# Kernel tuning notes

Hardware: AMD Instinct MI355X
Metric: run time of the kernel (lower is better)

Reference implementation:

```python
import jax, jax.numpy as jnp
import numpy as np

GAMMA = 1.0

def setup_inputs() -> dict:
    key = jax.random.key(0)
    kx, ky = jax.random.split(key)
    X = jax.random.normal(kx, (8192, 64), dtype=jnp.float32)
    Y = jax.random.normal(ky, (8192, 64), dtype=jnp.float32)
    return {"X": X, "Y": Y}

def reference(X, Y):
    x2 = jnp.sum(X * X, axis=-1)            # (n,)
    y2 = jnp.sum(Y * Y, axis=-1)            # (m,)
    xy = X @ Y.T                            # (n, m)
    dist2 = x2[:, None] + y2[None, :] - 2.0 * xy
    dist2 = jnp.maximum(dist2, 0.0)         # numerical guard
    return jnp.exp(-GAMMA * dist2)
```

## Files before the change

### kernel.cpp

```cpp
#include <hip/hip_runtime.h>

typedef __attribute__((ext_vector_type(8))) short          short8_t;
typedef __attribute__((ext_vector_type(8))) unsigned short ushort8_t;
typedef __attribute__((ext_vector_type(4))) float          floatx4;

constexpr int N_ROWS = 8192;
constexpr int DIM    = 64;
constexpr int TILE   = 128;
constexpr int PANEL  = TILE * DIM;

__device__ __forceinline__ unsigned short bf16_rne(float f) {
    unsigned int u = __float_as_uint(f);
    u += 0x7FFFu + ((u >> 16) & 1u);
    return (unsigned short)(u >> 16);
}

typedef __attribute__((address_space(1))) unsigned int gu32;
typedef __attribute__((address_space(3))) unsigned int lu32;
__device__ __forceinline__ void gload16(const void* g, void* l) {
    __builtin_amdgcn_global_load_lds((gu32*)g, (lu32*)l, 16, 0, 0);
}

__global__ void __launch_bounds__(256)
split_norms_kernel(const float* __restrict__ X, const float* __restrict__ Y,
                   float* __restrict__ x2, float* __restrict__ y2,
                   unsigned short* __restrict__ Xs, unsigned short* __restrict__ Ys) {
    const int r  = blockIdx.x * 256 + threadIdx.x;
    const int p  = r >> 7;
    const int rl = r & 127;
    const int swz = (rl & 7) * 8;
    const size_t pb = (size_t)p * (2 * PANEL);

    const float4* xr = reinterpret_cast<const float4*>(X + (size_t)r * DIM);
    const float4* yr = reinterpret_cast<const float4*>(Y + (size_t)r * DIM);

    float sx = 0.f, sy = 0.f;
#pragma unroll
    for (int c = 0; c < 8; ++c) {
        const int off = (rl * DIM + c * 8) ^ swz;
        float f[8];
        ushort8_t hi, lo;

        *reinterpret_cast<float4*>(&f[0]) = xr[2 * c];
        *reinterpret_cast<float4*>(&f[4]) = xr[2 * c + 1];
#pragma unroll
        for (int e = 0; e < 8; ++e) {
            sx = fmaf(f[e], f[e], sx);
            unsigned short hh = bf16_rne(f[e]);
            hi[e] = hh;
            lo[e] = bf16_rne(f[e] - __uint_as_float((unsigned int)hh << 16));
        }
        *reinterpret_cast<ushort8_t*>(&Xs[pb + off])         = hi;
        *reinterpret_cast<ushort8_t*>(&Xs[pb + PANEL + off]) = lo;

        *reinterpret_cast<float4*>(&f[0]) = yr[2 * c];
        *reinterpret_cast<float4*>(&f[4]) = yr[2 * c + 1];
#pragma unroll
        for (int e = 0; e < 8; ++e) {
            sy = fmaf(f[e], f[e], sy);
            unsigned short hh = bf16_rne(f[e]);
            hi[e] = hh;
            lo[e] = bf16_rne(f[e] - __uint_as_float((unsigned int)hh << 16));
        }
        *reinterpret_cast<ushort8_t*>(&Ys[pb + off])         = hi;
        *reinterpret_cast<ushort8_t*>(&Ys[pb + PANEL + off]) = lo;
    }
    x2[r] = sx;
    y2[r] = sy;
}

__global__ void __launch_bounds__(256, 2)
rbf_mfma_kernel(const unsigned short* __restrict__ Xs,
                const unsigned short* __restrict__ Ys,
                const float* __restrict__ x2, const float* __restrict__ y2,
                float* __restrict__ out) {
    __shared__ unsigned short smem[4 * PANEL];

    const int tid  = threadIdx.x;
    const int lane = tid & 63;
    const int w    = tid >> 6;
    const int row0 = blockIdx.y * TILE;
    const int col0 = blockIdx.x * TILE;

    {
        const unsigned short* src =
            (w < 2) ? Xs + (size_t)blockIdx.y * (2 * PANEL) + w * PANEL
                    : Ys + (size_t)blockIdx.x * (2 * PANEL) + (w & 1) * PANEL;
        unsigned short* dst = &smem[w * PANEL];
#pragma unroll
        for (int it = 0; it < 16; ++it)
            gload16(src + it * 512 + lane * 8, dst + it * 512);
    }
    __syncthreads();

    const int li = lane & 15;
    const int lg = lane >> 4;
    const int wr = (w >> 1) * 64;
    const int wc = (w & 1) * 64;

    floatx4 acc[4][4] = {};

#define LDF(qbase, rowbase, koff)                                              \
    (*reinterpret_cast<const short8_t*>(                                       \
        &smem[(qbase) + ((rowbase) + li) * DIM + (koff)]))

#pragma unroll
    for (int ks = 0; ks < 2; ++ks) {
        const int koff = (ks * 32 + lg * 8) ^ ((li & 7) * 8);
        short8_t aH[4], bH[4], aL[4], bL[4];
#pragma unroll
        for (int mi = 0; mi < 4; ++mi) aH[mi] = LDF(0 * PANEL, wr + mi * 16, koff);
#pragma unroll
        for (int ni = 0; ni < 4; ++ni) bH[ni] = LDF(2 * PANEL, wc + ni * 16, koff);
#pragma unroll
        for (int mi = 0; mi < 4; ++mi)
#pragma unroll
            for (int ni = 0; ni < 4; ++ni)
                acc[mi][ni] = __builtin_amdgcn_mfma_f32_16x16x32_bf16(
                    bH[ni], aH[mi], acc[mi][ni], 0, 0, 0);
#pragma unroll
        for (int ni = 0; ni < 4; ++ni) bL[ni] = LDF(3 * PANEL, wc + ni * 16, koff);
#pragma unroll
        for (int mi = 0; mi < 4; ++mi)
#pragma unroll
            for (int ni = 0; ni < 4; ++ni)
                acc[mi][ni] = __builtin_amdgcn_mfma_f32_16x16x32_bf16(
                    bL[ni], aH[mi], acc[mi][ni], 0, 0, 0);
#pragma unroll
        for (int mi = 0; mi < 4; ++mi) aL[mi] = LDF(1 * PANEL, wr + mi * 16, koff);
#pragma unroll
        for (int mi = 0; mi < 4; ++mi)
#pragma unroll
            for (int ni = 0; ni < 4; ++ni)
                acc[mi][ni] = __builtin_amdgcn_mfma_f32_16x16x32_bf16(
                    bH[ni], aL[mi], acc[mi][ni], 0, 0, 0);
    }
#undef LDF

    const int orow = row0 + wr + li;
    const int ocol = col0 + wc + lg * 4;
#pragma unroll
    for (int mi = 0; mi < 4; ++mi) {
        const float xs = x2[orow + mi * 16];
        float* obase = out + (size_t)(orow + mi * 16) * N_ROWS + ocol;
#pragma unroll
        for (int ni = 0; ni < 4; ++ni) {
            const float4 yv = *reinterpret_cast<const float4*>(&y2[ocol + ni * 16]);
            float4 o;
            o.x = __expf(-fmaxf(fmaf(-2.f, acc[mi][ni][0], xs + yv.x), 0.f));
            o.y = __expf(-fmaxf(fmaf(-2.f, acc[mi][ni][1], xs + yv.y), 0.f));
            o.z = __expf(-fmaxf(fmaf(-2.f, acc[mi][ni][2], xs + yv.z), 0.f));
            o.w = __expf(-fmaxf(fmaf(-2.f, acc[mi][ni][3], xs + yv.w), 0.f));
            *reinterpret_cast<float4*>(obase + ni * 16) = o;
        }
    }
}

extern "C" void kernel_launch(void* const* d_in, const int* in_sizes, int n_in,
                              void* d_out, int out_size, void* d_ws, size_t ws_size,
                              hipStream_t stream) {
    const float* X = (const float*)d_in[0];
    const float* Y = (const float*)d_in[1];
    float* out = (float*)d_out;

    float* x2 = (float*)d_ws;
    float* y2 = x2 + N_ROWS;
    unsigned short* Xs = (unsigned short*)(y2 + N_ROWS);
    unsigned short* Ys = Xs + (N_ROWS / TILE) * 2 * PANEL;

    split_norms_kernel<<<N_ROWS / 256, 256, 0, stream>>>(X, Y, x2, y2, Xs, Ys);

    dim3 grid(N_ROWS / TILE, N_ROWS / TILE);
    rbf_mfma_kernel<<<grid, 256, 0, stream>>>(Xs, Ys, x2, y2, out);
}
```

Before: 76.11 us.

## Pre-pack split bf16 operands in MFMA fragment order and load directly from global

The split kernel now writes the hi/lo bf16 panels in the exact per-lane MFMA fragment order and uses two threads per row, reducing the squared norm with a shuffle. The main kernel drops LDS staging and __syncthreads. It becomes a single-wave 64x64 block that reads fragments straight from global memory as coalesced 16-byte loads. This removes LDS traffic and barriers, at the cost of more global and L2 reads, since operand panels are no longer shared across four waves, and a four-times-larger grid.

```diff
diff --git a/kernel.cpp b/kernel.cpp
--- a/kernel.cpp
+++ b/kernel.cpp
@@ -6,8 +6,7 @@
 
 constexpr int N_ROWS = 8192;
 constexpr int DIM    = 64;
-constexpr int TILE   = 128;
-constexpr int PANEL  = TILE * DIM;
+constexpr int PANEL  = 128 * DIM;
 
 __device__ __forceinline__ unsigned short bf16_rne(float f) {
     unsigned int u = __float_as_uint(f);
@@ -15,29 +14,26 @@
     return (unsigned short)(u >> 16);
 }
 
-typedef __attribute__((address_space(1))) unsigned int gu32;
-typedef __attribute__((address_space(3))) unsigned int lu32;
-__device__ __forceinline__ void gload16(const void* g, void* l) {
-    __builtin_amdgcn_global_load_lds((gu32*)g, (lu32*)l, 16, 0, 0);
-}
-
 __global__ void __launch_bounds__(256)
 split_norms_kernel(const float* __restrict__ X, const float* __restrict__ Y,
                    float* __restrict__ x2, float* __restrict__ y2,
                    unsigned short* __restrict__ Xs, unsigned short* __restrict__ Ys) {
-    const int r  = blockIdx.x * 256 + threadIdx.x;
+    const int t  = blockIdx.x * 256 + threadIdx.x;
+    const int r  = t >> 1;
+    const int h  = t & 1;
     const int p  = r >> 7;
     const int rl = r & 127;
-    const int swz = (rl & 7) * 8;
+    const int g  = rl >> 4;
+    const int li = rl & 15;
     const size_t pb = (size_t)p * (2 * PANEL);
 
-    const float4* xr = reinterpret_cast<const float4*>(X + (size_t)r * DIM);
-    const float4* yr = reinterpret_cast<const float4*>(Y + (size_t)r * DIM);
+    const float4* xr = reinterpret_cast<const float4*>(X + (size_t)r * DIM + h * 32);
+    const float4* yr = reinterpret_cast<const float4*>(Y + (size_t)r * DIM + h * 32);
 
     float sx = 0.f, sy = 0.f;
 #pragma unroll
-    for (int c = 0; c < 8; ++c) {
-        const int off = (rl * DIM + c * 8) ^ swz;
+    for (int c = 0; c < 4; ++c) {
+        const int off = ((g * 2 + h) * 64 + c * 16 + li) * 8;
         float f[8];
         ushort8_t hi, lo;
 
@@ -65,53 +61,37 @@
         *reinterpret_cast<ushort8_t*>(&Ys[pb + off])         = hi;
         *reinterpret_cast<ushort8_t*>(&Ys[pb + PANEL + off]) = lo;
     }
-    x2[r] = sx;
-    y2[r] = sy;
+    sx += __shfl_xor(sx, 1);
+    sy += __shfl_xor(sy, 1);
+    if (h == 0) { x2[r] = sx; y2[r] = sy; }
 }
 
-__global__ void __launch_bounds__(256, 2)
+__global__ void __launch_bounds__(64)
 rbf_mfma_kernel(const unsigned short* __restrict__ Xs,
                 const unsigned short* __restrict__ Ys,
                 const float* __restrict__ x2, const float* __restrict__ y2,
                 float* __restrict__ out) {
-    __shared__ unsigned short smem[4 * PANEL];
-
-    const int tid  = threadIdx.x;
-    const int lane = tid & 63;
-    const int w    = tid >> 6;
-    const int row0 = blockIdx.y * TILE;
-    const int col0 = blockIdx.x * TILE;
-
-    {
-        const unsigned short* src =
-            (w < 2) ? Xs + (size_t)blockIdx.y * (2 * PANEL) + w * PANEL
-                    : Ys + (size_t)blockIdx.x * (2 * PANEL) + (w & 1) * PANEL;
-        unsigned short* dst = &smem[w * PANEL];
-#pragma unroll
-        for (int it = 0; it < 16; ++it)
-            gload16(src + it * 512 + lane * 8, dst + it * 512);
-    }
-    __syncthreads();
-
-    const int li = lane & 15;
-    const int lg = lane >> 4;
-    const int wr = (w >> 1) * 64;
-    const int wc = (w & 1) * 64;
+    const int lane = threadIdx.x;
+    const int row0 = blockIdx.y * 64;
+    const int col0 = blockIdx.x * 64;
+    const unsigned short* Xp = Xs + (size_t)(blockIdx.y >> 1) * (2 * PANEL);
+    const unsigned short* Yp = Ys + (size_t)(blockIdx.x >> 1) * (2 * PANEL);
+    const int gx0 = (blockIdx.y & 1) * 4;
+    const int gy0 = (blockIdx.x & 1) * 4;
 
     floatx4 acc[4][4] = {};
 
-#define LDF(qbase, rowbase, koff)                                              \
+#define GF(P, hl, g, ks)                                                       \
     (*reinterpret_cast<const short8_t*>(                                       \
-        &smem[(qbase) + ((rowbase) + li) * DIM + (koff)]))
+        (P) + (hl) * PANEL + (((g) * 2 + (ks)) * 64 + lane) * 8))
 
 #pragma unroll
     for (int ks = 0; ks < 2; ++ks) {
-        const int koff = (ks * 32 + lg * 8) ^ ((li & 7) * 8);
         short8_t aH[4], bH[4], aL[4], bL[4];
 #pragma unroll
-        for (int mi = 0; mi < 4; ++mi) aH[mi] = LDF(0 * PANEL, wr + mi * 16, koff);
+        for (int mi = 0; mi < 4; ++mi) aH[mi] = GF(Xp, 0, gx0 + mi, ks);
 #pragma unroll
-        for (int ni = 0; ni < 4; ++ni) bH[ni] = LDF(2 * PANEL, wc + ni * 16, koff);
+        for (int ni = 0; ni < 4; ++ni) bH[ni] = GF(Yp, 0, gy0 + ni, ks);
 #pragma unroll
         for (int mi = 0; mi < 4; ++mi)
 #pragma unroll
@@ -119,7 +99,7 @@
                 acc[mi][ni] = __builtin_amdgcn_mfma_f32_16x16x32_bf16(
                     bH[ni], aH[mi], acc[mi][ni], 0, 0, 0);
 #pragma unroll
-        for (int ni = 0; ni < 4; ++ni) bL[ni] = LDF(3 * PANEL, wc + ni * 16, koff);
+        for (int ni = 0; ni < 4; ++ni) bL[ni] = GF(Yp, 1, gy0 + ni, ks);
 #pragma unroll
         for (int mi = 0; mi < 4; ++mi)
 #pragma unroll
@@ -127,7 +107,7 @@
                 acc[mi][ni] = __builtin_amdgcn_mfma_f32_16x16x32_bf16(
                     bL[ni], aH[mi], acc[mi][ni], 0, 0, 0);
 #pragma unroll
-        for (int mi = 0; mi < 4; ++mi) aL[mi] = LDF(1 * PANEL, wr + mi * 16, koff);
+        for (int mi = 0; mi < 4; ++mi) aL[mi] = GF(Xp, 1, gx0 + mi, ks);
 #pragma unroll
         for (int mi = 0; mi < 4; ++mi)
 #pragma unroll
@@ -135,10 +115,12 @@
                 acc[mi][ni] = __builtin_amdgcn_mfma_f32_16x16x32_bf16(
                     bH[ni], aL[mi], acc[mi][ni], 0, 0, 0);
     }
-#undef LDF
+#undef GF
 
-    const int orow = row0 + wr + li;
-    const int ocol = col0 + wc + lg * 4;
+    const int li = lane & 15;
+    const int lg = lane >> 4;
+    const int orow = row0 + li;
+    const int ocol = col0 + lg * 4;
 #pragma unroll
     for (int mi = 0; mi < 4; ++mi) {
         const float xs = x2[orow + mi * 16];
@@ -166,10 +148,10 @@
     float* x2 = (float*)d_ws;
     float* y2 = x2 + N_ROWS;
     unsigned short* Xs = (unsigned short*)(y2 + N_ROWS);
-    unsigned short* Ys = Xs + (N_ROWS / TILE) * 2 * PANEL;
+    unsigned short* Ys = Xs + (N_ROWS / 128) * 2 * PANEL;
 
-    split_norms_kernel<<<N_ROWS / 256, 256, 0, stream>>>(X, Y, x2, y2, Xs, Ys);
+    split_norms_kernel<<<(2 * N_ROWS) / 256, 256, 0, stream>>>(X, Y, x2, y2, Xs, Ys);
 
-    dim3 grid(N_ROWS / TILE, N_ROWS / TILE);
-    rbf_mfma_kernel<<<grid, 256, 0, stream>>>(Xs, Ys, x2, y2, out);
+    dim3 grid(N_ROWS / 64, N_ROWS / 64);
+    rbf_mfma_kernel<<<grid, 64, 0, stream>>>(Xs, Ys, x2, y2, out);
 }
```

New measurement: 73.60 us. 3.3% less time.
